# Optimization experiments

Hardware: AMD Instinct MI355X
Metric: run time of the kernel (lower is better)

## Reference

```python
import jax, jax.numpy as jnp
import numpy as np


def conv2d(x, w, b):
    # x: [B,C,H,W], w: [O,I,5,5], VALID, stride 1 (matches torch Conv2d defaults)
    y = jax.lax.conv_general_dilated(x, w, (1, 1), 'VALID',
                                     dimension_numbers=('NCHW', 'OIHW', 'NCHW'))
    return y + b[None, :, None, None]


def maxpool_2x5(x):
    # MaxPool2d(kernel=(2,5), stride=(2,1))
    return jax.lax.reduce_window(x, -jnp.inf, jax.lax.max,
                                 (1, 1, 2, 5), (1, 1, 2, 1), 'VALID')


def gru(x, w_ih, w_hh, b_ih, b_hh):
    # Faithful torch nn.GRU (batch_first=False): x is [L, N, 64]; gate order r,z,n.
    H = w_hh.shape[1]
    h0 = jnp.zeros((x.shape[1], H), x.dtype)

    def step(h, xt):
        gi = xt @ w_ih.T + b_ih
        gh = h @ w_hh.T + b_hh
        i_r, i_z, i_n = jnp.split(gi, 3, axis=-1)
        h_r, h_z, h_n = jnp.split(gh, 3, axis=-1)
        r = jax.nn.sigmoid(i_r + h_r)
        z = jax.nn.sigmoid(i_z + h_z)
        n = jnp.tanh(i_n + r * h_n)
        h_new = (1.0 - z) * n + z * h
        return h_new, h_new

    _, ys = jax.lax.scan(step, h0, x)
    return ys


def branch(x, w1, b1, w2, b2, w3, b3, lw, lb, gwih, gwhh, gbih, gbhh):
    x = x[:, None]                      # [B,1,H,W]
    x = conv2d(x, w1, b1)
    x = conv2d(x, w2, b2)
    x = conv2d(x, w3, b3)
    x = maxpool_2x5(x)                  # [B,64,58,W']
    B = x.shape[0]
    x = x.reshape(B, x.shape[-1], 3712)  # same row-major reshape as torch
    x = x @ lw.T + lb                   # [B,W',64]
    # nn.GRU without batch_first scans over dim 0 (batch!) — replicate exactly
    return gru(x, gwih, gwhh, gbih, gbhh)


def _make_params(key):
    ks = iter(jax.random.split(key, 40))
    def p(shape, scale=0.05):
        return (jax.random.normal(next(ks), shape, jnp.float32) * scale)
    d = {}
    for pre in ('e', 't'):
        d[f'{pre}_w1'] = p((16, 1, 5, 5)); d[f'{pre}_b1'] = p((16,))
        d[f'{pre}_w2'] = p((32, 16, 5, 5)); d[f'{pre}_b2'] = p((32,))
        d[f'{pre}_w3'] = p((64, 32, 5, 5)); d[f'{pre}_b3'] = p((64,))
        d[f'{pre}l_w'] = p((64, 3712), 0.01); d[f'{pre}l_b'] = p((64,))
        d[f'{pre}g_wih'] = p((192, 64)); d[f'{pre}g_whh'] = p((192, 64))
        d[f'{pre}g_bih'] = p((192,)); d[f'{pre}g_bhh'] = p((192,))
    d['a_w'] = p((1, 64)); d['a_b'] = p((1,))
    d['h_w'] = p((128, 64)); d['h_b'] = p((128,))
    d['c_w'] = p((2, 128)); d['c_b'] = p((2,))
    return d


def setup_inputs() -> dict:
    key = jax.random.key(0)
    k1, k2, k3 = jax.random.split(key, 3)
    inp = {
        'evaluation': jax.random.normal(k1, (4, 128, 2048), jnp.float32),
        'template': jax.random.normal(k2, (4, 128, 1040), jnp.float32),
    }
    inp.update(_make_params(k3))
    return inp


def reference(evaluation, template,
              e_w1, e_b1, e_w2, e_b2, e_w3, e_b3, el_w, el_b,
              eg_wih, eg_whh, eg_bih, eg_bhh,
              t_w1, t_b1, t_w2, t_b2, t_w3, t_b3, tl_w, tl_b,
              tg_wih, tg_whh, tg_bih, tg_bhh,
              a_w, a_b, h_w, h_b, c_w, c_b):
    e = branch(evaluation, e_w1, e_b1, e_w2, e_b2, e_w3, e_b3,
               el_w, el_b, eg_wih, eg_whh, eg_bih, eg_bhh)   # [B,Se,64]
    t = branch(template, t_w1, t_b1, t_w2, t_b2, t_w3, t_b3,
               tl_w, tl_b, tg_wih, tg_whh, tg_bih, tg_bhh)   # [B,St,64]
    # bmm(template, eval^T) -> [B,St,Se], softmax over Se
    tt = jax.nn.softmax(jnp.einsum('btd,bed->bte', t, e), axis=-1)
    # bmm(tt^T, template) -> [B,Se,64]
    tt = jnp.einsum('bte,btd->bed', tt, t)
    tt = jnp.abs(tt - e)
    # attention over eval sequence positions
    att = jax.nn.softmax((e @ a_w.T + a_b)[..., 0], axis=-1)  # [B,Se]
    # vectorized form of the original Python double loop
    red = jnp.einsum('bed,be->bd', tt, att)                   # [B,64]
    h = jax.nn.relu(red @ h_w.T + h_b)
    return jax.nn.softmax(h @ c_w.T + c_b, axis=-1)           # [B,2]
```

## Files before the change

kernel.cpp:

```cpp
#include <hip/hip_runtime.h>
#include <hip/hip_bf16.h>
#include <cmath>


typedef unsigned short u16;
typedef unsigned int u32;
typedef __attribute__((ext_vector_type(8))) short bf16x8;
typedef __attribute__((ext_vector_type(8))) unsigned short u16x8;
typedef __attribute__((ext_vector_type(16))) float f32x16;

__device__ __forceinline__ u16 f2bf(float f) {
  unsigned int x = __float_as_uint(f);
  return (u16)((x + 0x7fffu + ((x >> 16) & 1u)) >> 16);
}
__device__ __forceinline__ float bf2f(u16 v) {
  return __uint_as_float(((unsigned int)v) << 16);
}
__device__ __forceinline__ u32 f2bf_pk(float a, float b) {
  __hip_bfloat162 h = __float22bfloat162_rn(float2{a, b});
  u32 r;
  __builtin_memcpy(&r, &h, 4);
  return r;
}

static const size_t OFF_BEFF_E  = 0;
static const size_t OFF_BEFF_T  = 64;
static const size_t OFF_BIAS2_E = 128;
static const size_t OFF_BIAS2_T = 320;
static const size_t OFF_WKX_E   = 512;
static const size_t OFF_WKX_T   = 27136;
static const size_t OFF_W12P_E  = 53760;
static const size_t OFF_W12P_T  = 63008;
static const size_t OFF_B12_E   = 72256;
static const size_t OFF_B12_T   = 72288;
static const size_t OFF_LWT1_E  = 72320;
static const size_t OFF_LWT1_T  = 191104;
static const size_t OFF_ATT     = 309888;
static const size_t OFF_XYBF_E  = 318016;
static const size_t OFF_XYBF_T  = 578112;
static const size_t OFF_TTBF    = 709184;
static const size_t OFF_LIN_E   = 840256;
static const size_t OFF_LIN_T   = 1360448;
static const size_t OFF_PV      = 1622592;
static const size_t OFF_RED     = 2142784;
static const size_t OFF_RSUM    = 2143040;
static const size_t ZERO_F4     = 326720;
static const size_t ZSTRIDE     = 617;
static const size_t OFF_GI_E    = 2147136;
static const size_t OFF_GI_T    = 3707712;
static const size_t OFF_P       = 4494144;

__global__ __launch_bounds__(320) void prep_kernel(
    const float* __restrict__ w1e, const float* __restrict__ b1e,
    const float* __restrict__ w2e, const float* __restrict__ b2e,
    const float* __restrict__ w1t, const float* __restrict__ b1t,
    const float* __restrict__ w2t, const float* __restrict__ b2t,
    float* __restrict__ w12p_e, float* __restrict__ w12p_t,
    float* __restrict__ b12o_e, float* __restrict__ b12o_t,
    const float* __restrict__ wih_e, const float* __restrict__ bih_e,
    const float* __restrict__ lb_e, float* __restrict__ bias2_e,
    const float* __restrict__ wih_t, const float* __restrict__ bih_t,
    const float* __restrict__ lb_t, float* __restrict__ bias2_t,
    const float* __restrict__ lwe, const float* __restrict__ lwt,
    u16* __restrict__ lwt1_e, u16* __restrict__ lwt1_t,
    float4* __restrict__ zbase) {
  const int bx = blockIdx.x;
  const int tid = threadIdx.x;
  {
    const size_t base = (size_t)bx * ZSTRIDE;
    const float4 z = {0.f, 0.f, 0.f, 0.f};
    for (size_t i = base + tid; i < base + ZSTRIDE && i < ZERO_F4; i += 320)
      zbase[i] = z;
  }
  if (bx >= 66) {
    if (tid < 256) {
      const int k = bx - 66;
      const int br = k / 232, j = k - br * 232;
      const float* src = br ? lwt : lwe;
      u16* dst = br ? lwt1_t : lwt1_e;
      const int e = j * 1024 + tid * 4;
      const int h = e >> 12;
      const int rem = e & 4095;
      const int n = rem >> 6, c = rem & 63;
      const float* s = src + (size_t)n * 3712 + (size_t)c * 58 + h;
      const float v0 = s[0], v1 = s[58], v2 = s[116], v3 = s[174];
      *(u32*)&dst[e] = f2bf_pk(v0, v1);
      *(u32*)&dst[e + 2] = f2bf_pk(v2, v3);
    }
    return;
  }
  if (bx >= 64) {
    const int br = bx - 64;
    const float* wih = br ? wih_t : wih_e;
    const float* bih = br ? bih_t : bih_e;
    const float* lb = br ? lb_t : lb_e;
    float* bias2 = br ? bias2_t : bias2_e;
    __shared__ float s_lb[64];
    if (tid < 64) s_lb[tid] = lb[tid];
    __syncthreads();
    if (tid < 192) {
      float acc = bih[tid];
      const float* wr = wih + tid * 64;
      for (int d = 0; d < 64; ++d) acc = fmaf(wr[d], s_lb[d], acc);
      bias2[tid] = acc;
    }
    return;
  }
  const int br = bx >> 5;
  const float* w1 = br ? w1t : w1e;
  const float* b1 = br ? b1t : b1e;
  const float* w2 = br ? w2t : w2e;
  const float* b2 = br ? b2t : b2e;
  float* w12p = br ? w12p_t : w12p_e;
  float* b12o = br ? b12o_t : b12o_e;
  const int c12 = bx & 31;
  __shared__ float s_w1pad[16 * 169];
  __shared__ float s_w2c[400];
  __shared__ float s_b1[16];
  for (int i = tid; i < 2704; i += 320) s_w1pad[i] = 0.f;
  if (tid < 16) s_b1[tid] = b1[tid];
  __syncthreads();
  for (int i = tid; i < 400; i += 320) {
    const int c1 = i / 25, r = (i % 25) / 5, cc = i % 5;
    s_w1pad[c1 * 169 + (r + 4) * 13 + (cc + 4)] = w1[i];
    s_w2c[i] = w2[c12 * 400 + i];
  }
  __syncthreads();
  if (tid < 289) {
    const int py = tid / 17, px = tid % 17;
    float v = 0.f;
    if (py >= 4 && py <= 12 && px >= 4 && px <= 12) {
      const int sy = py - 4, sx = px - 4;
      float accs[2] = {0.f, 0.f};
      for (int c1 = 0; c1 < 16; ++c1) {
        const float* w2p = s_w2c + c1 * 25;
        const float* w1p = s_w1pad + c1 * 169 + (sy + 4) * 13 + (sx + 4);
#pragma unroll
        for (int uy = 0; uy < 5; ++uy)
#pragma unroll
          for (int ux = 0; ux < 5; ++ux)
            accs[uy & 1] = fmaf(w2p[uy * 5 + ux], w1p[-(uy * 13) - ux], accs[uy & 1]);
      }
      v = accs[0] + accs[1];
    }
    w12p[c12 * 289 + tid] = v;
  } else if (tid == 300) {
    float acc = b2[c12];
    for (int c1 = 0; c1 < 16; ++c1) {
      float sw = 0.f;
      for (int u = 0; u < 25; ++u) sw += s_w2c[c1 * 25 + u];
      acc = fmaf(sw, s_b1[c1], acc);
    }
    b12o[c12] = acc;
  }
}

__global__ __launch_bounds__(256) void compose_weff_kernel(
    const float* __restrict__ w3e, const float* __restrict__ b3e,
    const float* __restrict__ w3t, const float* __restrict__ b3t,
    const float* __restrict__ w12p_e, const float* __restrict__ w12p_t,
    const float* __restrict__ b12_e, const float* __restrict__ b12_t,
    u16* __restrict__ wkx_e, u16* __restrict__ wkx_t,
    float* __restrict__ beff_e, float* __restrict__ beff_t) {
  const int br = blockIdx.y;
  const float* w3 = br ? w3t : w3e;
  const float* b3 = br ? b3t : b3e;
  const float* w12p = br ? w12p_t : w12p_e;
  const float* b12 = br ? b12_t : b12_e;
  u16* wkx = br ? wkx_t : wkx_e;
  float* beff = br ? beff_t : beff_e;
  const int o = blockIdx.x;
  __shared__ float s_pad[32 * 289];
  __shared__ float s_w3o[800];
  __shared__ float s_b12[32];
  const int tid = threadIdx.x;
  for (int i = tid; i < 9248; i += 256) s_pad[i] = w12p[i];
  for (int i = tid; i < 800; i += 256) s_w3o[i] = w3[o * 800 + i];
  if (tid < 32) s_b12[tid] = b12[tid];
  __syncthreads();
  if (tid < 169) {
    const int sy = tid / 13, sx = tid % 13;
    float accs[4] = {0.f, 0.f, 0.f, 0.f};
#pragma unroll 4
    for (int c = 0; c < 32; ++c) {
      const float* w3p = s_w3o + c * 25;
      const float* wp = s_pad + c * 289 + (sy + 4) * 17 + (sx + 4);
#pragma unroll
      for (int uy = 0; uy < 5; ++uy)
#pragma unroll
        for (int ux = 0; ux < 5; ++ux)
          accs[c & 3] = fmaf(w3p[uy * 5 + ux], wp[-(uy * 17) - ux], accs[c & 3]);
    }
    const u16 v = f2bf(accs[0] + accs[1] + accs[2] + accs[3]);
#pragma unroll
    for (int p = 0; p < 4; ++p)
      wkx[((p * 13 + sx) * 64 + o) * 16 + sy + p] = v;
  } else if (tid < 169 + 156) {
    const int t = tid - 169, kx = t / 12, q = t % 12;
    const int p = q / 3, idx = q % 3;
    const int slot = (idx < p) ? idx : (p + 13) + (idx - p);
    wkx[((p * 13 + kx) * 64 + o) * 16 + slot] = 0;
  }
  if (tid == 255) {
    float acc = b3[o];
    for (int c = 0; c < 32; ++c) {
      float sw = 0.f;
      for (int u = 0; u < 25; ++u) sw += s_w3o[c * 25 + u];
      acc = fmaf(sw, s_b12[c], acc);
    }
    beff[o] = acc;
  }
}

__global__ __launch_bounds__(256, 3) void conv_pool_lin_kernel(
    const float* __restrict__ xe, const u16* __restrict__ wkx_e,
    const float* __restrict__ beff_e, const u16* __restrict__ lwt1_e,
    float* __restrict__ lin_e,
    const float* __restrict__ xt, const u16* __restrict__ wkx_t,
    const float* __restrict__ beff_t, const u16* __restrict__ lwt1_t,
    float* __restrict__ lin_t) {
  const int zz = blockIdx.z;
  const bool ev = zz < 4;
  const int b = ev ? zz : zz - 4;
  const int W = ev ? 2048 : 1040;
  const int T = ev ? 2032 : 1024;
  const int cb = blockIdx.x * 60;
  if (cb >= T) return;
  const float* x = ev ? xe : xt;
  const u16* wkx = ev ? wkx_e : wkx_t;
  const float* beff = ev ? beff_e : beff_t;
  const u16* lwt1 = ev ? lwt1_e : lwt1_t;
  float* lin = ev ? lin_e : lin_t;

  __shared__ __align__(16) u16 s_x[80 * 24];
  __shared__ __align__(16) u16 s_out[2 * 64 * 66];
  __shared__ __align__(16) u16 s_poolT[64 * 72];

  const int tid = threadIdx.x;
  const int lane = tid & 63, wave = tid >> 6;
  const int rsel = wave & 1, cm = (wave >> 1) * 32;
  const int l31 = lane & 31, g8 = (lane >> 5) * 8;
  const int th = (wave & 1) * 32, nh = (wave >> 1) * 32;

  const int by0 = blockIdx.y * 3;
  const int by1 = (by0 + 3 < 29) ? (by0 + 3) : 29;

  f32x16 accL = {};
  for (int by = by0; by < by1; ++by) {
    const int r0 = 4 * by;
    {
      const float* xb = x + ((size_t)b * 128 + r0) * W;
      for (int i = tid; i < 640; i += 256) {
        const int pr = i / 80, c = i - pr * 80;
        int gc = cb + c;
        if (gc > W - 1) gc = W - 1;
        *(u32*)&s_x[c * 24 + 2 * pr] =
            f2bf_pk(xb[(size_t)(2 * pr) * W + gc], xb[(size_t)(2 * pr + 1) * W + gc]);
      }
    }
    __syncthreads();
#pragma unroll
    for (int hh = 0; hh < 2; ++hh) {
      const int p = 2 * hh + rsel;
      const int h = 2 * by + hh;
      const u16* aw = wkx + ((p * 13) * 64 + cm + l31) * 16 + g8;
      f32x16 acc0 = {}, acc1 = {};
      const u16* bx = s_x + g8;
#pragma unroll
      for (int kx = 0; kx < 13; ++kx) {
        const bf16x8 w = *(const bf16x8*)(aw + kx * 1024);
        bf16x8 b0 = *(const bf16x8*)(bx + (l31 + kx) * 24);
        bf16x8 b1 = *(const bf16x8*)(bx + (32 + l31 + kx) * 24);
        acc0 = __builtin_amdgcn_mfma_f32_32x32x16_bf16(w, b0, acc0, 0, 0, 0);
        acc1 = __builtin_amdgcn_mfma_f32_32x32x16_bf16(w, b1, acc1, 0, 0, 0);
      }
#pragma unroll
      for (int r = 0; r < 16; ++r) {
        const int c = cm + (r & 3) + 8 * (r >> 2) + (g8 >> 1);
        u16* o = s_out + (rsel * 64 + c) * 66;
        const u32 pk = f2bf_pk(acc0[r], acc1[r]);
        o[l31] = (u16)pk;
        o[32 + l31] = (u16)(pk >> 16);
      }
      __syncthreads();
      {
        const int pc = tid & 63, tg = tid >> 6;
        const int t0 = tg * 15;
        const float bias = beff[pc];
        const u16* r0p = s_out + pc * 66 + t0;
        const u16* r1p = s_out + (64 + pc) * 66 + t0;
        float m01[19];
#pragma unroll
        for (int j = 0; j < 19; ++j) m01[j] = fmaxf(bf2f(r0p[j]), bf2f(r1p[j]));
#pragma unroll
        for (int i = 0; i < 15; ++i) {
          float m = m01[i];
#pragma unroll
          for (int k = 1; k < 5; ++k) m = fmaxf(m, m01[i + k]);
          s_poolT[(t0 + i) * 72 + pc] = f2bf(m + bias);
        }
      }
      __syncthreads();
      {
        const u16* ap2 = s_poolT + (th + l31) * 72 + g8;
        const u16* bp2 = lwt1 + ((size_t)(h * 64 + nh + l31)) * 64 + g8;
#pragma unroll
        for (int ks = 0; ks < 4; ++ks) {
          bf16x8 a = *(const bf16x8*)(ap2 + ks * 16);
          bf16x8 bb = *(const bf16x8*)(bp2 + ks * 16);
          accL = __builtin_amdgcn_mfma_f32_32x32x16_bf16(a, bb, accL, 0, 0, 0);
        }
      }
    }
  }
  {
    const int nn = nh + l31;
#pragma unroll
    for (int r = 0; r < 16; ++r) {
      const int t = th + (r & 3) + 8 * (r >> 2) + (g8 >> 1);
      const int tt = cb + t;
      if (t < 60 && tt < T)
        atomicAdd(&lin[((size_t)b * T + tt) * 64 + nn], accL[r]);
    }
  }
}

__global__ __launch_bounds__(256) void gemm_gi_kernel(
    const float* __restrict__ Ae, const float* __restrict__ Wte,
    const float* __restrict__ biase, float* __restrict__ oute,
    const float* __restrict__ At, const float* __restrict__ Wtt,
    const float* __restrict__ biast, float* __restrict__ outt) {
  const int bx = blockIdx.x;
  const bool ev = bx < 127;
  const float* A = ev ? Ae : At;
  const float* Wt = ev ? Wte : Wtt;
  const float* bias = ev ? biase : biast;
  float* out = ev ? oute : outt;
  const int r0 = (ev ? bx : bx - 127) * 64;
  const int N = 192, K = 64;
  __shared__ float sA[64 * 33];
  __shared__ float sB[64 * 33];
  const int tid = threadIdx.x;
  const int n0 = blockIdx.y * 64;
  const int ty = tid >> 4, tx = tid & 15;
  float acc[4][4] = {};
  for (int kc = 0; kc < K; kc += 32) {
    __syncthreads();
#pragma unroll
    for (int rep = 0; rep < 8; ++rep) {
      const int l = tid + rep * 256;
      const int row = l >> 5, kk = l & 31;
      sA[row * 33 + kk] = A[(size_t)(r0 + row) * K + kc + kk];
      sB[row * 33 + kk] = Wt[(size_t)(n0 + row) * K + kc + kk];
    }
    __syncthreads();
#pragma unroll 8
    for (int kk = 0; kk < 32; ++kk) {
      const float a0 = sA[(ty * 4 + 0) * 33 + kk];
      const float a1 = sA[(ty * 4 + 1) * 33 + kk];
      const float a2 = sA[(ty * 4 + 2) * 33 + kk];
      const float a3 = sA[(ty * 4 + 3) * 33 + kk];
      const float b0 = sB[(tx * 4 + 0) * 33 + kk];
      const float b1 = sB[(tx * 4 + 1) * 33 + kk];
      const float b2 = sB[(tx * 4 + 2) * 33 + kk];
      const float b3 = sB[(tx * 4 + 3) * 33 + kk];
      acc[0][0] = fmaf(a0, b0, acc[0][0]); acc[0][1] = fmaf(a0, b1, acc[0][1]);
      acc[0][2] = fmaf(a0, b2, acc[0][2]); acc[0][3] = fmaf(a0, b3, acc[0][3]);
      acc[1][0] = fmaf(a1, b0, acc[1][0]); acc[1][1] = fmaf(a1, b1, acc[1][1]);
      acc[1][2] = fmaf(a1, b2, acc[1][2]); acc[1][3] = fmaf(a1, b3, acc[1][3]);
      acc[2][0] = fmaf(a2, b0, acc[2][0]); acc[2][1] = fmaf(a2, b1, acc[2][1]);
      acc[2][2] = fmaf(a2, b2, acc[2][2]); acc[2][3] = fmaf(a2, b3, acc[2][3]);
      acc[3][0] = fmaf(a3, b0, acc[3][0]); acc[3][1] = fmaf(a3, b1, acc[3][1]);
      acc[3][2] = fmaf(a3, b2, acc[3][2]); acc[3][3] = fmaf(a3, b3, acc[3][3]);
    }
  }
#pragma unroll
  for (int i = 0; i < 4; ++i)
#pragma unroll
    for (int j = 0; j < 4; ++j)
      out[(size_t)(r0 + ty * 4 + i) * N + n0 + tx * 4 + j] =
          acc[i][j] + bias[n0 + tx * 4 + j];
}

__global__ __launch_bounds__(256) void gru_rec_kernel(
    float* __restrict__ xyE, const float* __restrict__ giE,
    const float* __restrict__ whhE, const float* __restrict__ bhhE,
    float* __restrict__ xyT, const float* __restrict__ giT,
    const float* __restrict__ whhT, const float* __restrict__ bhhT,
    u16* __restrict__ xybfE, u16* __restrict__ xybfT, u16* __restrict__ ttbf,
    const float* __restrict__ a_w, const float* __restrict__ a_b,
    float* __restrict__ logits) {
  const int bxid = blockIdx.x;
  const bool ev = bxid < 127;
  float* xy = ev ? xyE : xyT;
  u16* xybf = ev ? xybfE : xybfT;
  const float* gi = ev ? giE : giT;
  const float* whh = ev ? whhE : whhT;
  const float* bhh = ev ? bhhE : bhhT;
  const int T = ev ? 2032 : 1024;
  const int t0 = (ev ? bxid : bxid - 127) * 16;
  __shared__ float s_whh_t[64 * 192];
  __shared__ float s_h[16][64];
  __shared__ float s_aw[64];
  const int tid = threadIdx.x;
  const int lane = tid & 63, wave = tid >> 6;
  for (int i = tid; i < 192 * 64; i += 256) {
    const int j = i >> 6, d = i & 63;
    s_whh_t[d * 192 + j] = whh[i];
  }
  for (int i = tid; i < 16 * 64; i += 256) (&s_h[0][0])[i] = 0.f;
  if (tid < 64) s_aw[tid] = a_w[tid];
  const float ab = a_b[0];
  const float bhr = bhh[lane], bhz = bhh[64 + lane], bhn = bhh[128 + lane];
  __syncthreads();
  for (int b = 0; b < 4; ++b) {
    float gir[4], giz[4], gin[4];
#pragma unroll
    for (int sl = 0; sl < 4; ++sl) {
      int t = t0 + wave * 4 + sl; if (t > T - 1) t = T - 1;
      const float* girow = gi + ((size_t)b * T + t) * 192;
      gir[sl] = girow[lane]; giz[sl] = girow[64 + lane]; gin[sl] = girow[128 + lane];
    }
    float ahr[4] = {}, ahz[4] = {}, ahn[4] = {};
    for (int d = 0; d < 64; ++d) {
      const float wr_ = s_whh_t[d * 192 + lane];
      const float wz_ = s_whh_t[d * 192 + 64 + lane];
      const float wn_ = s_whh_t[d * 192 + 128 + lane];
#pragma unroll
      for (int sl = 0; sl < 4; ++sl) {
        const float hv = s_h[wave * 4 + sl][d];
        ahr[sl] = fmaf(wr_, hv, ahr[sl]);
        ahz[sl] = fmaf(wz_, hv, ahz[sl]);
        ahn[sl] = fmaf(wn_, hv, ahn[sl]);
      }
    }
    float hn[4];
#pragma unroll
    for (int sl = 0; sl < 4; ++sl) {
      const float r = 1.f / (1.f + __expf(-(gir[sl] + ahr[sl] + bhr)));
      const float z = 1.f / (1.f + __expf(-(giz[sl] + ahz[sl] + bhz)));
      const float n = tanhf(gin[sl] + r * (ahn[sl] + bhn));
      hn[sl] = (1.f - z) * n + z * s_h[wave * 4 + sl][lane];
    }
    __syncthreads();
#pragma unroll
    for (int sl = 0; sl < 4; ++sl) {
      const int t = t0 + wave * 4 + sl;
      s_h[wave * 4 + sl][lane] = hn[sl];
      if (t < T) {
        const size_t idx = ((size_t)b * T + t) * 64 + lane;
        xy[idx] = hn[sl];
        xybf[idx] = f2bf(hn[sl]);
        if (ev) {
          float v = hn[sl] * s_aw[lane];
#pragma unroll
          for (int off = 32; off > 0; off >>= 1) v += __shfl_down(v, off, 64);
          if (lane == 0) logits[b * 2032 + t] = v + ab;
        } else {
          ttbf[((size_t)b * 64 + lane) * 1024 + t] = f2bf(hn[sl]);
        }
      }
    }
    __syncthreads();
  }
}

__global__ __launch_bounds__(256) void scores_mfma_kernel(
    const u16* __restrict__ tbf, const u16* __restrict__ ebf,
    u16* __restrict__ P, float* __restrict__ rowsum) {
  __shared__ __align__(16) u16 sA[64 * 72];
  __shared__ __align__(16) u16 sB[128 * 72];
  const int tid = threadIdx.x;
  const int b = blockIdx.z;
  const int tau0 = blockIdx.x * 64;
  const int e0 = blockIdx.y * 128;
  const int lane = tid & 63, wave = tid >> 6;
  const int l31 = lane & 31, g8 = (lane >> 5) * 8;
  {
    const int row = tid >> 2, seg = (tid & 3) * 16;
    const u16* ap = &tbf[((size_t)b * 1024 + tau0 + row) * 64 + seg];
    u16* da = &sA[row * 72 + seg];
    *(u16x8*)da = *(const u16x8*)ap;
    *(u16x8*)(da + 8) = *(const u16x8*)(ap + 8);
  }
#pragma unroll
  for (int r = 0; r < 4; ++r) {
    const int q = tid + r * 256;
    const int row = q >> 3, seg = (q & 7) * 8;
    int eps = e0 + row; if (eps > 2031) eps = 2031;
    *(u16x8*)&sB[row * 72 + seg] =
        *(const u16x8*)&ebf[((size_t)b * 2032 + eps) * 64 + seg];
  }
  __syncthreads();
  const int mh = (wave & 1) * 32;
  const int nq = (wave >> 1) * 64;
  f32x16 acc0 = {}, acc1 = {};
#pragma unroll
  for (int ks = 0; ks < 4; ++ks) {
    bf16x8 a = *(const bf16x8*)&sA[(mh + l31) * 72 + ks * 16 + g8];
    bf16x8 b0 = *(const bf16x8*)&sB[(nq + l31) * 72 + ks * 16 + g8];
    bf16x8 b1 = *(const bf16x8*)&sB[(nq + 32 + l31) * 72 + ks * 16 + g8];
    acc0 = __builtin_amdgcn_mfma_f32_32x32x16_bf16(a, b0, acc0, 0, 0, 0);
    acc1 = __builtin_amdgcn_mfma_f32_32x32x16_bf16(a, b1, acc1, 0, 0, 0);
  }
  const int ep0 = e0 + nq + l31;
  const int ep1 = ep0 + 32;
#pragma unroll
  for (int r = 0; r < 16; ++r) {
    const int tau = tau0 + mh + (r & 3) + 8 * (r >> 2) + (g8 >> 1);
    const size_t prow = ((size_t)b * 1024 + tau) * 2032;
    const float e0v = __expf(acc0[r]);
    const float e1v = __expf(acc1[r]);
    float part = 0.f;
    if (ep0 < 2032) { P[prow + ep0] = f2bf(e0v); part += e0v; }
    if (ep1 < 2032) { P[prow + ep1] = f2bf(e1v); part += e1v; }
#pragma unroll
    for (int off = 16; off > 0; off >>= 1) part += __shfl_down(part, off, 32);
    if (l31 == 0) atomicAdd(&rowsum[b * 1024 + tau], part);
  }
}

__global__ __launch_bounds__(256) void pv_mfma_kernel(
    const u16* __restrict__ P, const u16* __restrict__ ttbf,
    const float* __restrict__ rowsum, float* __restrict__ PV) {
  __shared__ __align__(16) u16 sPT[64 * 72];
  __shared__ __align__(16) u16 sTT[64 * 72];
  const int tid = threadIdx.x;
  const int b = blockIdx.z;
  const int e0 = blockIdx.x * 64;
  const int tau_base = blockIdx.y * 256;
  const int lane = tid & 63, wave = tid >> 6;
  const int l31 = lane & 31, g8 = (lane >> 5) * 8;
  const int mh = (wave & 1) * 32, nh = (wave >> 1) * 32;
  f32x16 acc = {};
  for (int cc = 0; cc < 4; ++cc) {
    const int tc = tau_base + cc * 64;
    __syncthreads();
#pragma unroll
    for (int k = 0; k < 2; ++k) {
      const int q = tid + k * 256;
      const int row = q >> 3, seg = (q & 7) * 8;
      const float inv = 1.0f / rowsum[b * 1024 + tc + row];
      int er = e0 + seg;
      if (er > 2032 - 8) er = 2032 - 8;
      const u16x8 v = *(const u16x8*)&P[((size_t)b * 1024 + tc + row) * 2032 + er];
#pragma unroll
      for (int j = 0; j < 8; ++j)
        sPT[(seg + j) * 72 + row] = f2bf(bf2f(v[j]) * inv);
    }
#pragma unroll
    for (int k = 0; k < 2; ++k) {
      const int q = tid + k * 256;
      const int row = q >> 3, seg = (q & 7) * 8;
      *(u16x8*)&sTT[row * 72 + seg] =
          *(const u16x8*)&ttbf[((size_t)b * 64 + row) * 1024 + tc + seg];
    }
    __syncthreads();
#pragma unroll
    for (int ks = 0; ks < 4; ++ks) {
      bf16x8 a = *(const bf16x8*)&sPT[(mh + l31) * 72 + ks * 16 + g8];
      bf16x8 bb = *(const bf16x8*)&sTT[(nh + l31) * 72 + ks * 16 + g8];
      acc = __builtin_amdgcn_mfma_f32_32x32x16_bf16(a, bb, acc, 0, 0, 0);
    }
  }
#pragma unroll
  for (int r = 0; r < 16; ++r) {
    const int eps = e0 + mh + (r & 3) + 8 * (r >> 2) + (g8 >> 1);
    if (eps < 2032)
      atomicAdd(&PV[((size_t)b * 2032 + eps) * 64 + nh + l31], acc[r]);
  }
}

__global__ __launch_bounds__(256) void red_reduce_kernel(
    const float* __restrict__ emat, const float* __restrict__ PV,
    const float* __restrict__ logits, float* __restrict__ red) {
  __shared__ float s_att[2032];
  __shared__ float sred[4];
  __shared__ float s_part[4][64];
  const int tid = threadIdx.x;
  const int lane = tid & 63, wave = tid >> 6;
  const int b = blockIdx.y;
  float m = -3.4e38f;
  for (int i = tid; i < 2032; i += 256) {
    const float v = logits[b * 2032 + i];
    s_att[i] = v;
    m = fmaxf(m, v);
  }
#pragma unroll
  for (int off = 32; off > 0; off >>= 1) m = fmaxf(m, __shfl_down(m, off, 64));
  if (lane == 0) sred[wave] = m;
  __syncthreads();
  m = fmaxf(fmaxf(sred[0], sred[1]), fmaxf(sred[2], sred[3]));
  __syncthreads();
  float ssum = 0.f;
  for (int i = tid; i < 2032; i += 256) {
    const float v = __expf(s_att[i] - m);
    s_att[i] = v;
    ssum += v;
  }
#pragma unroll
  for (int off = 32; off > 0; off >>= 1) ssum += __shfl_down(ssum, off, 64);
  if (lane == 0) sred[wave] = ssum;
  __syncthreads();
  const float inv = 1.f / (sred[0] + sred[1] + sred[2] + sred[3]);
  const int i0 = blockIdx.x * 127;
  float acc = 0.f;
  for (int i = i0 + wave; i < i0 + 127; i += 4) {
    const size_t idx = ((size_t)b * 2032 + i) * 64 + lane;
    acc = fmaf(fabsf(PV[idx] - emat[idx]), s_att[i], acc);
  }
  s_part[wave][lane] = acc;
  __syncthreads();
  if (tid < 64)
    atomicAdd(&red[b * 64 + tid],
              (s_part[0][tid] + s_part[1][tid] + s_part[2][tid] + s_part[3][tid]) * inv);
}

__global__ __launch_bounds__(128) void mlp_kernel(
    const float* __restrict__ red, const float* __restrict__ h_w,
    const float* __restrict__ h_b, const float* __restrict__ c_w,
    const float* __restrict__ c_b, float* __restrict__ out) {
  __shared__ float s_red[64];
  __shared__ float s_hv[128];
  const int tid = threadIdx.x;
  const int b = blockIdx.x;
  if (tid < 64) s_red[tid] = red[b * 64 + tid];
  __syncthreads();
  {
    float acc = h_b[tid];
    const float* hw = h_w + tid * 64;
    for (int d = 0; d < 64; ++d) acc = fmaf(s_red[d], hw[d], acc);
    s_hv[tid] = fmaxf(acc, 0.f);
  }
  __syncthreads();
  if (tid == 0) {
    float l0 = c_b[0], l1 = c_b[1];
    for (int j = 0; j < 128; ++j) {
      l0 = fmaf(s_hv[j], c_w[j], l0);
      l1 = fmaf(s_hv[j], c_w[128 + j], l1);
    }
    const float mm = fmaxf(l0, l1);
    const float e0 = __expf(l0 - mm), e1 = __expf(l1 - mm);
    const float invs = 1.f / (e0 + e1);
    out[b * 2 + 0] = e0 * invs;
    out[b * 2 + 1] = e1 * invs;
  }
}

extern "C" void kernel_launch(void* const* d_in, const int* in_sizes, int n_in,
                              void* d_out, int out_size, void* d_ws, size_t ws_size,
                              hipStream_t stream) {
  const float* evaluation = (const float*)d_in[0];
  const float* templ      = (const float*)d_in[1];
  const float* e_w1 = (const float*)d_in[2];
  const float* e_b1 = (const float*)d_in[3];
  const float* e_w2 = (const float*)d_in[4];
  const float* e_b2 = (const float*)d_in[5];
  const float* e_w3 = (const float*)d_in[6];
  const float* e_b3 = (const float*)d_in[7];
  const float* el_w = (const float*)d_in[8];
  const float* el_b = (const float*)d_in[9];
  const float* eg_wih = (const float*)d_in[10];
  const float* eg_whh = (const float*)d_in[11];
  const float* eg_bih = (const float*)d_in[12];
  const float* eg_bhh = (const float*)d_in[13];
  const float* t_w1 = (const float*)d_in[14];
  const float* t_b1 = (const float*)d_in[15];
  const float* t_w2 = (const float*)d_in[16];
  const float* t_b2 = (const float*)d_in[17];
  const float* t_w3 = (const float*)d_in[18];
  const float* t_b3 = (const float*)d_in[19];
  const float* tl_w = (const float*)d_in[20];
  const float* tl_b = (const float*)d_in[21];
  const float* tg_wih = (const float*)d_in[22];
  const float* tg_whh = (const float*)d_in[23];
  const float* tg_bih = (const float*)d_in[24];
  const float* tg_bhh = (const float*)d_in[25];
  const float* a_w = (const float*)d_in[26];
  const float* a_b = (const float*)d_in[27];
  const float* h_w = (const float*)d_in[28];
  const float* h_b = (const float*)d_in[29];
  const float* c_w = (const float*)d_in[30];
  const float* c_b = (const float*)d_in[31];

  float* ws = (float*)d_ws;
  float* beff_e  = ws + OFF_BEFF_E;
  float* beff_t  = ws + OFF_BEFF_T;
  float* bias2_e = ws + OFF_BIAS2_E;
  float* bias2_t = ws + OFF_BIAS2_T;
  u16*   wkx_e   = (u16*)(ws + OFF_WKX_E);
  u16*   wkx_t   = (u16*)(ws + OFF_WKX_T);
  float* w12p_e  = ws + OFF_W12P_E;
  float* w12p_t  = ws + OFF_W12P_T;
  float* b12_e   = ws + OFF_B12_E;
  float* b12_t   = ws + OFF_B12_T;
  u16*   lwt1_e  = (u16*)(ws + OFF_LWT1_E);
  u16*   lwt1_t  = (u16*)(ws + OFF_LWT1_T);
  float* attbuf  = ws + OFF_ATT;
  u16*   xybf_e  = (u16*)(ws + OFF_XYBF_E);
  u16*   xybf_t  = (u16*)(ws + OFF_XYBF_T);
  u16*   ttbf    = (u16*)(ws + OFF_TTBF);
  float* lin_e   = ws + OFF_LIN_E;
  float* lin_t   = ws + OFF_LIN_T;
  float* PVbuf   = ws + OFF_PV;
  float* redbuf  = ws + OFF_RED;
  float* rsum    = ws + OFF_RSUM;
  float* gi_e    = ws + OFF_GI_E;
  float* gi_t    = ws + OFF_GI_T;
  u16*   Pbuf    = (u16*)(ws + OFF_P);

  prep_kernel<<<530, 320, 0, stream>>>(
      e_w1, e_b1, e_w2, e_b2, t_w1, t_b1, t_w2, t_b2, w12p_e, w12p_t, b12_e, b12_t,
      eg_wih, eg_bih, el_b, bias2_e, tg_wih, tg_bih, tl_b, bias2_t,
      el_w, tl_w, lwt1_e, lwt1_t, (float4*)lin_e);
  compose_weff_kernel<<<dim3(64, 2), 256, 0, stream>>>(
      e_w3, e_b3, t_w3, t_b3, w12p_e, w12p_t, b12_e, b12_t, wkx_e, wkx_t, beff_e, beff_t);

  conv_pool_lin_kernel<<<dim3(34, 10, 8), 256, 0, stream>>>(
      evaluation, wkx_e, beff_e, lwt1_e, lin_e,
      templ, wkx_t, beff_t, lwt1_t, lin_t);
  gemm_gi_kernel<<<dim3(191, 3), 256, 0, stream>>>(
      lin_e, eg_wih, bias2_e, gi_e, lin_t, tg_wih, bias2_t, gi_t);
  gru_rec_kernel<<<191, 256, 0, stream>>>(
      lin_e, gi_e, eg_whh, eg_bhh, lin_t, gi_t, tg_whh, tg_bhh,
      xybf_e, xybf_t, ttbf, a_w, a_b, attbuf);

  scores_mfma_kernel<<<dim3(16, 16, 4), 256, 0, stream>>>(xybf_t, xybf_e, Pbuf, rsum);
  pv_mfma_kernel<<<dim3(32, 4, 4), 256, 0, stream>>>(Pbuf, ttbf, rsum, PVbuf);

  red_reduce_kernel<<<dim3(16, 4), 256, 0, stream>>>(lin_e, PVbuf, attbuf, redbuf);
  mlp_kernel<<<4, 128, 0, stream>>>(redbuf, h_w, h_b, c_w, c_b, (float*)d_out);
}
```

Baseline: 311.3 us.

## Prefetch conv and linear weights, split MFMA chains, vectorize pooling reads

The fused conv/pool/linear kernel now loads all 13 conv weight fragments and the linear-weight fragments into registers before the MFMA loop. The 13-step accumulation is split into two independent accumulator chains so MFMAs can issue back to back instead of waiting on each other. The s_out row stride is padded to 72 so the pooling stage can use 16-byte vector LDS reads, and the bias is cached in shared memory. In exchange, register pressure rises and launch bounds drop from 3 to 2 blocks per SM, which lowers occupancy.

```diff
diff --git a/kernel.cpp b/kernel.cpp
--- a/kernel.cpp
+++ b/kernel.cpp
@@ -212,7 +212,7 @@
   }
 }
 
-__global__ __launch_bounds__(256, 3) void conv_pool_lin_kernel(
+__global__ __launch_bounds__(256, 2) void conv_pool_lin_kernel(
     const float* __restrict__ xe, const u16* __restrict__ wkx_e,
     const float* __restrict__ beff_e, const u16* __restrict__ lwt1_e,
     float* __restrict__ lin_e,
@@ -233,14 +233,17 @@
   float* lin = ev ? lin_e : lin_t;
 
   __shared__ __align__(16) u16 s_x[80 * 24];
-  __shared__ __align__(16) u16 s_out[2 * 64 * 66];
+  __shared__ __align__(16) u16 s_out[2 * 64 * 72];
   __shared__ __align__(16) u16 s_poolT[64 * 72];
+  __shared__ float s_beff[64];
 
   const int tid = threadIdx.x;
   const int lane = tid & 63, wave = tid >> 6;
   const int rsel = wave & 1, cm = (wave >> 1) * 32;
   const int l31 = lane & 31, g8 = (lane >> 5) * 8;
   const int th = (wave & 1) * 32, nh = (wave >> 1) * 32;
+
+  if (tid < 64) s_beff[tid] = beff[tid];
 
   const int by0 = blockIdx.y * 3;
   const int by1 = (by0 + 3 < 29) ? (by0 + 3) : 29;
@@ -263,52 +266,82 @@
     for (int hh = 0; hh < 2; ++hh) {
       const int p = 2 * hh + rsel;
       const int h = 2 * by + hh;
-      const u16* aw = wkx + ((p * 13) * 64 + cm + l31) * 16 + g8;
-      f32x16 acc0 = {}, acc1 = {};
-      const u16* bx = s_x + g8;
-#pragma unroll
-      for (int kx = 0; kx < 13; ++kx) {
-        const bf16x8 w = *(const bf16x8*)(aw + kx * 1024);
-        bf16x8 b0 = *(const bf16x8*)(bx + (l31 + kx) * 24);
-        bf16x8 b1 = *(const bf16x8*)(bx + (32 + l31 + kx) * 24);
-        acc0 = __builtin_amdgcn_mfma_f32_32x32x16_bf16(w, b0, acc0, 0, 0, 0);
-        acc1 = __builtin_amdgcn_mfma_f32_32x32x16_bf16(w, b1, acc1, 0, 0, 0);
+      bf16x8 wfrag[13];
+      {
+        const u16* aw = wkx + ((p * 13) * 64 + cm + l31) * 16 + g8;
+#pragma unroll
+        for (int kx = 0; kx < 13; ++kx) wfrag[kx] = *(const bf16x8*)(aw + kx * 1024);
+      }
+      bf16x8 bb[4];
+      {
+        const u16* bp2 = lwt1 + ((size_t)(h * 64 + nh + l31)) * 64 + g8;
+#pragma unroll
+        for (int ks = 0; ks < 4; ++ks) bb[ks] = *(const bf16x8*)(bp2 + ks * 16);
+      }
+      f32x16 c0a = {}, c1a = {}, c0b = {}, c1b = {};
+      const u16* bxp = s_x + g8;
+#pragma unroll
+      for (int kx = 0; kx < 6; ++kx) {
+        bf16x8 b0 = *(const bf16x8*)(bxp + (l31 + kx) * 24);
+        bf16x8 b1 = *(const bf16x8*)(bxp + (32 + l31 + kx) * 24);
+        bf16x8 b0q = *(const bf16x8*)(bxp + (l31 + kx + 7) * 24);
+        bf16x8 b1q = *(const bf16x8*)(bxp + (32 + l31 + kx + 7) * 24);
+        c0a = __builtin_amdgcn_mfma_f32_32x32x16_bf16(wfrag[kx], b0, c0a, 0, 0, 0);
+        c1a = __builtin_amdgcn_mfma_f32_32x32x16_bf16(wfrag[kx], b1, c1a, 0, 0, 0);
+        c0b = __builtin_amdgcn_mfma_f32_32x32x16_bf16(wfrag[kx + 7], b0q, c0b, 0, 0, 0);
+        c1b = __builtin_amdgcn_mfma_f32_32x32x16_bf16(wfrag[kx + 7], b1q, c1b, 0, 0, 0);
+      }
+      {
+        bf16x8 b0 = *(const bf16x8*)(bxp + (l31 + 6) * 24);
+        bf16x8 b1 = *(const bf16x8*)(bxp + (32 + l31 + 6) * 24);
+        c0a = __builtin_amdgcn_mfma_f32_32x32x16_bf16(wfrag[6], b0, c0a, 0, 0, 0);
+        c1a = __builtin_amdgcn_mfma_f32_32x32x16_bf16(wfrag[6], b1, c1a, 0, 0, 0);
       }
 #pragma unroll
       for (int r = 0; r < 16; ++r) {
         const int c = cm + (r & 3) + 8 * (r >> 2) + (g8 >> 1);
-        u16* o = s_out + (rsel * 64 + c) * 66;
-        const u32 pk = f2bf_pk(acc0[r], acc1[r]);
+        u16* o = s_out + (rsel * 64 + c) * 72;
+        const u32 pk = f2bf_pk(c0a[r] + c0b[r], c1a[r] + c1b[r]);
         o[l31] = (u16)pk;
         o[32 + l31] = (u16)(pk >> 16);
       }
       __syncthreads();
       {
         const int pc = tid & 63, tg = tid >> 6;
-        const int t0 = tg * 15;
-        const float bias = beff[pc];
-        const u16* r0p = s_out + pc * 66 + t0;
-        const u16* r1p = s_out + (64 + pc) * 66 + t0;
-        float m01[19];
-#pragma unroll
-        for (int j = 0; j < 19; ++j) m01[j] = fmaxf(bf2f(r0p[j]), bf2f(r1p[j]));
-#pragma unroll
-        for (int i = 0; i < 15; ++i) {
-          float m = m01[i];
-#pragma unroll
-          for (int k = 1; k < 5; ++k) m = fmaxf(m, m01[i + k]);
-          s_poolT[(t0 + i) * 72 + pc] = f2bf(m + bias);
+        const int t0 = tg * 16;
+        const float bias = s_beff[pc];
+        const u16* r0p = s_out + pc * 72 + t0;
+        const u16* r1p = s_out + (64 + pc) * 72 + t0;
+        const u16x8 a0 = *(const u16x8*)(r0p);
+        const u16x8 a1 = *(const u16x8*)(r0p + 8);
+        const u16x8 a2 = *(const u16x8*)(r0p + 16);
+        const u16x8 q0 = *(const u16x8*)(r1p);
+        const u16x8 q1 = *(const u16x8*)(r1p + 8);
+        const u16x8 q2 = *(const u16x8*)(r1p + 16);
+        float m01[20];
+#pragma unroll
+        for (int j = 0; j < 8; ++j) {
+          m01[j] = fmaxf(bf2f(a0[j]), bf2f(q0[j]));
+          m01[j + 8] = fmaxf(bf2f(a1[j]), bf2f(q1[j]));
+          if (j < 4) m01[j + 16] = fmaxf(bf2f(a2[j]), bf2f(q2[j]));
+        }
+#pragma unroll
+        for (int i = 0; i < 16; ++i) {
+          if (t0 + i < 60) {
+            float m = m01[i];
+#pragma unroll
+            for (int k = 1; k < 5; ++k) m = fmaxf(m, m01[i + k]);
+            s_poolT[(t0 + i) * 72 + pc] = f2bf(m + bias);
+          }
         }
       }
       __syncthreads();
       {
         const u16* ap2 = s_poolT + (th + l31) * 72 + g8;
-        const u16* bp2 = lwt1 + ((size_t)(h * 64 + nh + l31)) * 64 + g8;
 #pragma unroll
         for (int ks = 0; ks < 4; ++ks) {
           bf16x8 a = *(const bf16x8*)(ap2 + ks * 16);
-          bf16x8 bb = *(const bf16x8*)(bp2 + ks * 16);
-          accL = __builtin_amdgcn_mfma_f32_32x32x16_bf16(a, bb, accL, 0, 0, 0);
+          accL = __builtin_amdgcn_mfma_f32_32x32x16_bf16(a, bb[ks], accL, 0, 0, 0);
         }
       }
     }
```

Measured after the change: 305.3 us. Within noise of the previous version (-1.9%).

## Restructure conv-pool-linear to fuse vertical max in registers and batch both rows

Applied to the files above, without the earlier changes.

Each wave now computes the two vertically pooled conv rows (p=2hh and 2hh+1) for the same channel and time tile, so the 2-row max is taken in registers before the store to LDS. Both pooled rows per block-row are handled together with double LDS buffers, which cuts the barriers per block-row from seven to three. The linear-layer weights are prefetched into registers before the conv, and bias is staged in LDS. The cost is more LDS and registers, and occupancy drops from three to two blocks per CU.

```diff
diff --git a/kernel.cpp b/kernel.cpp
--- a/kernel.cpp
+++ b/kernel.cpp
@@ -212,7 +212,7 @@
   }
 }
 
-__global__ __launch_bounds__(256, 3) void conv_pool_lin_kernel(
+__global__ __launch_bounds__(256, 2) void conv_pool_lin_kernel(
     const float* __restrict__ xe, const u16* __restrict__ wkx_e,
     const float* __restrict__ beff_e, const u16* __restrict__ lwt1_e,
     float* __restrict__ lin_e,
@@ -233,14 +233,17 @@
   float* lin = ev ? lin_e : lin_t;
 
   __shared__ __align__(16) u16 s_x[80 * 24];
-  __shared__ __align__(16) u16 s_out[2 * 64 * 66];
-  __shared__ __align__(16) u16 s_poolT[64 * 72];
+  __shared__ __align__(16) u16 s_m01[2][64 * 72];
+  __shared__ __align__(16) u16 s_poolT[2][64 * 72];
+  __shared__ float s_beff[64];
 
   const int tid = threadIdx.x;
   const int lane = tid & 63, wave = tid >> 6;
-  const int rsel = wave & 1, cm = (wave >> 1) * 32;
+  const int cm = (wave & 1) * 32, tm = (wave >> 1) * 32;
   const int l31 = lane & 31, g8 = (lane >> 5) * 8;
   const int th = (wave & 1) * 32, nh = (wave >> 1) * 32;
+
+  if (tid < 64) s_beff[tid] = beff[tid];
 
   const int by0 = blockIdx.y * 3;
   const int by1 = (by0 + 3 < 29) ? (by0 + 3) : 29;
@@ -258,58 +261,71 @@
             f2bf_pk(xb[(size_t)(2 * pr) * W + gc], xb[(size_t)(2 * pr + 1) * W + gc]);
       }
     }
-    __syncthreads();
+    bf16x8 bb[2][4];
 #pragma unroll
     for (int hh = 0; hh < 2; ++hh) {
-      const int p = 2 * hh + rsel;
-      const int h = 2 * by + hh;
-      const u16* aw = wkx + ((p * 13) * 64 + cm + l31) * 16 + g8;
-      f32x16 acc0 = {}, acc1 = {};
-      const u16* bx = s_x + g8;
+      const u16* bp2 = lwt1 + ((size_t)((2 * by + hh) * 64 + nh + l31)) * 64 + g8;
+#pragma unroll
+      for (int ks = 0; ks < 4; ++ks) bb[hh][ks] = *(const bf16x8*)(bp2 + ks * 16);
+    }
+    __syncthreads();
+#pragma unroll
+    for (int hh = 0; hh < 2; ++hh) {
+      const u16* aw0 = wkx + (((2 * hh) * 13) * 64 + cm + l31) * 16 + g8;
+      const u16* aw1 = wkx + (((2 * hh + 1) * 13) * 64 + cm + l31) * 16 + g8;
+      f32x16 a0 = {}, a1 = {};
+      const u16* bxp = s_x + g8 + tm * 24;
 #pragma unroll
       for (int kx = 0; kx < 13; ++kx) {
-        const bf16x8 w = *(const bf16x8*)(aw + kx * 1024);
-        bf16x8 b0 = *(const bf16x8*)(bx + (l31 + kx) * 24);
-        bf16x8 b1 = *(const bf16x8*)(bx + (32 + l31 + kx) * 24);
-        acc0 = __builtin_amdgcn_mfma_f32_32x32x16_bf16(w, b0, acc0, 0, 0, 0);
-        acc1 = __builtin_amdgcn_mfma_f32_32x32x16_bf16(w, b1, acc1, 0, 0, 0);
+        const bf16x8 bvec = *(const bf16x8*)(bxp + (l31 + kx) * 24);
+        const bf16x8 w0 = *(const bf16x8*)(aw0 + kx * 1024);
+        const bf16x8 w1 = *(const bf16x8*)(aw1 + kx * 1024);
+        a0 = __builtin_amdgcn_mfma_f32_32x32x16_bf16(w0, bvec, a0, 0, 0, 0);
+        a1 = __builtin_amdgcn_mfma_f32_32x32x16_bf16(w1, bvec, a1, 0, 0, 0);
       }
 #pragma unroll
       for (int r = 0; r < 16; ++r) {
         const int c = cm + (r & 3) + 8 * (r >> 2) + (g8 >> 1);
-        u16* o = s_out + (rsel * 64 + c) * 66;
-        const u32 pk = f2bf_pk(acc0[r], acc1[r]);
-        o[l31] = (u16)pk;
-        o[32 + l31] = (u16)(pk >> 16);
+        s_m01[hh][c * 72 + tm + l31] = f2bf(fmaxf(a0[r], a1[r]));
       }
-      __syncthreads();
-      {
-        const int pc = tid & 63, tg = tid >> 6;
-        const int t0 = tg * 15;
-        const float bias = beff[pc];
-        const u16* r0p = s_out + pc * 66 + t0;
-        const u16* r1p = s_out + (64 + pc) * 66 + t0;
-        float m01[19];
-#pragma unroll
-        for (int j = 0; j < 19; ++j) m01[j] = fmaxf(bf2f(r0p[j]), bf2f(r1p[j]));
-#pragma unroll
-        for (int i = 0; i < 15; ++i) {
-          float m = m01[i];
-#pragma unroll
-          for (int k = 1; k < 5; ++k) m = fmaxf(m, m01[i + k]);
-          s_poolT[(t0 + i) * 72 + pc] = f2bf(m + bias);
+    }
+    __syncthreads();
+    {
+      const int pc = tid & 63, tg = tid >> 6;
+      const int t0 = tg * 16;
+      const float bias = s_beff[pc];
+#pragma unroll
+      for (int hh = 0; hh < 2; ++hh) {
+        const u16* rp = &s_m01[hh][pc * 72 + t0];
+        const u16x8 v0 = *(const u16x8*)(rp);
+        const u16x8 v1 = *(const u16x8*)(rp + 8);
+        const u16x8 v2 = *(const u16x8*)(rp + 16);
+        float mv[20];
+#pragma unroll
+        for (int j = 0; j < 8; ++j) {
+          mv[j] = bf2f(v0[j]);
+          mv[j + 8] = bf2f(v1[j]);
+          if (j < 4) mv[j + 16] = bf2f(v2[j]);
+        }
+#pragma unroll
+        for (int i = 0; i < 16; ++i) {
+          if (t0 + i < 60) {
+            float m = mv[i];
+#pragma unroll
+            for (int k = 1; k < 5; ++k) m = fmaxf(m, mv[i + k]);
+            s_poolT[hh][(t0 + i) * 72 + pc] = f2bf(m + bias);
+          }
         }
       }
-      __syncthreads();
-      {
-        const u16* ap2 = s_poolT + (th + l31) * 72 + g8;
-        const u16* bp2 = lwt1 + ((size_t)(h * 64 + nh + l31)) * 64 + g8;
-#pragma unroll
-        for (int ks = 0; ks < 4; ++ks) {
-          bf16x8 a = *(const bf16x8*)(ap2 + ks * 16);
-          bf16x8 bb = *(const bf16x8*)(bp2 + ks * 16);
-          accL = __builtin_amdgcn_mfma_f32_32x32x16_bf16(a, bb, accL, 0, 0, 0);
-        }
+    }
+    __syncthreads();
+#pragma unroll
+    for (int hh = 0; hh < 2; ++hh) {
+      const u16* ap2 = &s_poolT[hh][(th + l31) * 72 + g8];
+#pragma unroll
+      for (int ks = 0; ks < 4; ++ks) {
+        const bf16x8 a = *(const bf16x8*)(ap2 + ks * 16);
+        accL = __builtin_amdgcn_mfma_f32_32x32x16_bf16(a, bb[hh][ks], accL, 0, 0, 0);
       }
     }
   }
```

New measurement: 386.5 us. 1.24x slower.
